# Performance work log

Measured on AMD Instinct MI355X. Metric: run time of the kernel, lower is better.

## Reference

```python
import jax, jax.numpy as jnp
import numpy as np

EPS = 1e-8
SIM_THRESHOLD = 0.5


def _conv(x, src, dst, W, b):
    # Gather per-edge endpoint features: x_j = source, x_i = target (PyG default flow)
    x_j = x[src]
    x_i = x[dst]
    # Cosine similarity per edge
    dot = jnp.sum(x_i * x_j, axis=1)
    denom = jnp.maximum(jnp.linalg.norm(x_i, axis=1) * jnp.linalg.norm(x_j, axis=1), EPS)
    sim = dot / denom
    mask = (sim > SIM_THRESHOLD).astype(x.dtype)[:, None]
    msg = x_j * mask
    # Scatter-add aggregate into target nodes
    agg = jax.ops.segment_sum(msg, dst, num_segments=x.shape[0])
    # update: Linear
    return agg @ W.T + b


def setup_inputs() -> dict:
    key = jax.random.key(0)
    k1, k2, k3, k4, k5 = jax.random.split(key, 5)
    N, E, D_IN, D_HID, D_OUT = 50000, 800000, 128, 256, 64
    x = jax.random.normal(k1, (N, D_IN), dtype=jnp.float32)
    edge_index = jax.random.randint(k2, (2, E), 0, N, dtype=jnp.int64)
    # Xavier-uniform linear weights, zero-ish bias
    lim1 = float(np.sqrt(6.0 / (D_IN + D_HID)))
    lim2 = float(np.sqrt(6.0 / (D_HID + D_OUT)))
    W1 = jax.random.uniform(k3, (D_HID, D_IN), minval=-lim1, maxval=lim1, dtype=jnp.float32)
    b1 = jnp.zeros((D_HID,), dtype=jnp.float32)
    W2 = jax.random.uniform(k4, (D_OUT, D_HID), minval=-lim2, maxval=lim2, dtype=jnp.float32)
    b2 = jnp.zeros((D_OUT,), dtype=jnp.float32)
    return {"x": x, "edge_index": edge_index, "W1": W1, "b1": b1, "W2": W2, "b2": b2}


def reference(x, edge_index, W1, b1, W2, b2):
    N = x.shape[0]
    # add self-loops
    loops = jnp.arange(N, dtype=edge_index.dtype)
    src = jnp.concatenate([edge_index[0], loops])
    dst = jnp.concatenate([edge_index[1], loops])
    h = _conv(x, src, dst, W1, b1)
    h = jax.nn.relu(h)  # dropout is identity in eval mode
    out = _conv(h, src, dst, W2, b2)
    return jax.nn.log_softmax(out, axis=-1)
```

## Files before the change

kernel.cpp:

```cpp
#include <hip/hip_runtime.h>
#include <math.h>

#define EPS 1e-8f
#define NB_SORT 256

#if defined(__has_builtin)
#if __has_builtin(__builtin_amdgcn_sdot4)
#define HAVE_SDOT4 1
#endif
#endif

typedef __attribute__((ext_vector_type(8))) short bf16x8;
typedef __attribute__((ext_vector_type(4))) float f32x4;

__device__ __forceinline__ int sdot4i(int a, int b, int c) {
#ifdef HAVE_SDOT4
  return __builtin_amdgcn_sdot4(a, b, c, false);
#else
  return c + ((int)(signed char)(a)) * ((int)(signed char)(b)) +
         ((int)(signed char)(a >> 8)) * ((int)(signed char)(b >> 8)) +
         ((int)(signed char)(a >> 16)) * ((int)(signed char)(b >> 16)) +
         (a >> 24) * (b >> 24);
#endif
}

__device__ __forceinline__ float wave_reduce_sum(float v) {
#pragma unroll
  for (int off = 32; off > 0; off >>= 1)
    v += __shfl_xor(v, off, 64);
  return v;
}

__device__ __forceinline__ float wave_reduce_max(float v) {
#pragma unroll
  for (int off = 32; off > 0; off >>= 1)
    v = fmaxf(v, __shfl_xor(v, off, 64));
  return v;
}

__device__ __forceinline__ float dot4(float4 a, float4 b) {
  return a.x * b.x + a.y * b.y + a.z * b.z + a.w * b.w;
}

__device__ __forceinline__ int clampq(float q) {
  int i = (int)rintf(q);
  return i < -127 ? -127 : (i > 127 ? 127 : i);
}

__device__ __forceinline__ void split_bf16(float x, unsigned int& hi,
                                           unsigned int& lo) {
  unsigned int u = __float_as_uint(x);
  hi = u >> 16;
  float hf = __uint_as_float(u & 0xFFFF0000u);
  float r = x - hf;
  lo = __float_as_uint(r) >> 16;
}

__device__ __forceinline__ void split8(float4 a0, float4 a1, bf16x8& th,
                                       bf16x8& tl) {
  unsigned int hh[8], ll[8];
  split_bf16(a0.x, hh[0], ll[0]); split_bf16(a0.y, hh[1], ll[1]);
  split_bf16(a0.z, hh[2], ll[2]); split_bf16(a0.w, hh[3], ll[3]);
  split_bf16(a1.x, hh[4], ll[4]); split_bf16(a1.y, hh[5], ll[5]);
  split_bf16(a1.z, hh[6], ll[6]); split_bf16(a1.w, hh[7], ll[7]);
#pragma unroll
  for (int j = 0; j < 8; ++j) {
    th[j] = (short)hh[j];
    tl[j] = (short)ll[j];
  }
}

__global__ __launch_bounds__(256) void hist_coarse(const int* __restrict__ dst,
                                                   int* __restrict__ hist_blk,
                                                   int E, int nbuck) {
  __shared__ int lh[1024];
  int t = threadIdx.x, blk = blockIdx.x;
  for (int i = t; i < nbuck; i += 256) lh[i] = 0;
  __syncthreads();
  int ch = (E + NB_SORT - 1) / NB_SORT;
  int lo = blk * ch, hi = min(E, lo + ch);
  for (int e = lo + t; e < hi; e += 256) atomicAdd(&lh[dst[e] >> 6], 1);
  __syncthreads();
  for (int i = t; i < nbuck; i += 256) hist_blk[i * NB_SORT + blk] = lh[i];
}

__global__ __launch_bounds__(256) void scan_local(int* __restrict__ hist,
                                                  int* __restrict__ bsum,
                                                  int nb) {
  __shared__ int tsum[256];
  int t = threadIdx.x;
  int base = blockIdx.x * 1024 + t * 4;
  int v0 = 0, v1 = 0, v2 = 0, v3 = 0;
  if (base + 3 < nb) {
    int4 q = *(const int4*)&hist[base];
    v0 = q.x; v1 = q.y; v2 = q.z; v3 = q.w;
  } else {
    if (base + 0 < nb) v0 = hist[base + 0];
    if (base + 1 < nb) v1 = hist[base + 1];
    if (base + 2 < nb) v2 = hist[base + 2];
  }
  tsum[t] = v0 + v1 + v2 + v3;
  __syncthreads();
  for (int off = 1; off < 256; off <<= 1) {
    int u = 0;
    if (t >= off) u = tsum[t - off];
    __syncthreads();
    if (t >= off) tsum[t] += u;
    __syncthreads();
  }
  int excl = (t == 0) ? 0 : tsum[t - 1];
  int e0 = excl, e1 = excl + v0, e2 = e1 + v1, e3 = e2 + v2;
  if (base + 3 < nb) {
    *(int4*)&hist[base] = make_int4(e0, e1, e2, e3);
  } else {
    if (base + 0 < nb) hist[base + 0] = e0;
    if (base + 1 < nb) hist[base + 1] = e1;
    if (base + 2 < nb) hist[base + 2] = e2;
  }
  if (t == 255) bsum[blockIdx.x] = tsum[255];
}

__global__ __launch_bounds__(256) void scan_bsum(int* __restrict__ bsum,
                                                 int nblk) {
  __shared__ int sh[256];
  int t = threadIdx.x;
  sh[t] = (t < nblk) ? bsum[t] : 0;
  __syncthreads();
  for (int off = 1; off < 256; off <<= 1) {
    int u = 0;
    if (t >= off) u = sh[t - off];
    __syncthreads();
    if (t >= off) sh[t] += u;
    __syncthreads();
  }
  if (t < nblk) bsum[t] = (t == 0) ? 0 : sh[t - 1];
}

__global__ __launch_bounds__(256) void add_bsum(int* __restrict__ hist,
                                                const int* __restrict__ bsum,
                                                int nb) {
  int i = blockIdx.x * blockDim.x + threadIdx.x;
  if (i < nb) hist[i] += bsum[i >> 10];
}

__global__ __launch_bounds__(256) void scatter_coarse(
    const int* __restrict__ src, const int* __restrict__ dst,
    const int* __restrict__ S, int2* __restrict__ epair, int E, int nbuck) {
  __shared__ int lb[1024];
  int t = threadIdx.x, blk = blockIdx.x;
  for (int i = t; i < nbuck; i += 256) lb[i] = S[i * NB_SORT + blk];
  __syncthreads();
  int ch = (E + NB_SORT - 1) / NB_SORT;
  int lo = blk * ch, hi = min(E, lo + ch);
  for (int e = lo + t; e < hi; e += 256) {
    int d = dst[e];
    int pos = atomicAdd(&lb[d >> 6], 1);
    epair[pos] = make_int2(src[e], d);
  }
}

__global__ __launch_bounds__(256) void fine_sort(
    const int2* __restrict__ epair, const int* __restrict__ S,
    int2* __restrict__ spair, int E, int nbuck) {
  __shared__ int fh[64];
  __shared__ int cur[64];
  int b = blockIdx.x, t = threadIdx.x;
  int bstart = S[b * NB_SORT];
  int bend = (b + 1 < nbuck) ? S[(b + 1) * NB_SORT] : E;
  if (t < 64) fh[t] = 0;
  __syncthreads();
  for (int e = bstart + t; e < bend; e += 256)
    atomicAdd(&fh[epair[e].y & 63], 1);
  __syncthreads();
  if (t < 64) {
    int v = fh[t];
    int incl = v;
#pragma unroll
    for (int off = 1; off < 64; off <<= 1) {
      int u = __shfl_up(incl, off, 64);
      if (t >= off) incl += u;
    }
    cur[t] = incl - v;
  }
  __syncthreads();
  for (int e = bstart + t; e < bend; e += 256) {
    int2 p = epair[e];
    int pos = atomicAdd(&cur[p.y & 63], 1);
    spair[bstart + pos] = p;
  }
}

__global__ __launch_bounds__(256) void prep_x(const float* __restrict__ x,
                                              signed char* __restrict__ qx,
                                              float4* __restrict__ nprop,
                                              float* __restrict__ agg,
                                              int N) {
  int node = (int)((blockIdx.x * blockDim.x + threadIdx.x) >> 6);
  int lane = threadIdx.x & 63;
  if (node >= N) return;
  float2 v = *(const float2*)(x + (size_t)node * 128 + lane * 2);
  float ax = fabsf(v.x), ay = fabsf(v.y);
  float mx = wave_reduce_max(fmaxf(ax, ay));
  float l1 = wave_reduce_sum(ax + ay);
  float ss = wave_reduce_sum(v.x * v.x + v.y * v.y);
  float s = mx * (1.0f / 127.0f);
  float inv = (mx > 0.f) ? 127.0f / mx : 0.f;
  int q0 = clampq(v.x * inv), q1 = clampq(v.y * inv);
  unsigned short w = (unsigned short)((q0 & 0xff) | ((q1 & 0xff) << 8));
  ((unsigned short*)(qx + (size_t)node * 128))[lane] = w;
  float l1q = s * wave_reduce_sum((float)(abs(q0) + abs(q1)));
  bool sp = ss > 0.5f * fmaxf(ss, EPS);
  *(float2*)(agg + (size_t)node * 128 + lane * 2) =
      sp ? v : make_float2(0.f, 0.f);
  if (lane == 0)
    nprop[node] = make_float4(sqrtf(ss), s, fmaxf(l1, l1q), 0.f);
}

__global__ __launch_bounds__(256) void prep_h(const float* __restrict__ h,
                                              signed char* __restrict__ qh,
                                              float4* __restrict__ nprop,
                                              float* __restrict__ agg,
                                              int N) {
  int node = (int)((blockIdx.x * blockDim.x + threadIdx.x) >> 6);
  int lane = threadIdx.x & 63;
  if (node >= N) return;
  float4 v = *(const float4*)(h + (size_t)node * 256 + lane * 4);
  float ax = fabsf(v.x), ay = fabsf(v.y), az = fabsf(v.z), aw = fabsf(v.w);
  float mx = wave_reduce_max(fmaxf(fmaxf(ax, ay), fmaxf(az, aw)));
  float l1 = wave_reduce_sum(ax + ay + az + aw);
  float ss = wave_reduce_sum(dot4(v, v));
  float s = mx * (1.0f / 127.0f);
  float inv = (mx > 0.f) ? 127.0f / mx : 0.f;
  int q0 = clampq(v.x * inv), q1 = clampq(v.y * inv);
  int q2 = clampq(v.z * inv), q3 = clampq(v.w * inv);
  int w = (q0 & 0xff) | ((q1 & 0xff) << 8) | ((q2 & 0xff) << 16) | (q3 << 24);
  ((int*)(qh + (size_t)node * 256))[lane] = w;
  float l1q = s * wave_reduce_sum((float)(abs(q0) + abs(q1) + abs(q2) + abs(q3)));
  bool sp = ss > 0.5f * fmaxf(ss, EPS);
  *(float4*)(agg + (size_t)node * 256 + lane * 4) =
      sp ? v : make_float4(0.f, 0.f, 0.f, 0.f);
  if (lane == 0)
    nprop[node] = make_float4(sqrtf(ss), s, fmaxf(l1, l1q), 0.f);
}

template <int D>
__global__ __launch_bounds__(256) void conv_coop(
    const float* __restrict__ xf, const signed char* __restrict__ qt,
    const float4* __restrict__ nprop, const int2* __restrict__ spair,
    float* __restrict__ agg, int E) {
  constexpr int G = D / 16;
  constexpr int EPW = 64 / G;
  constexpr int V = D / 64;
  const int tid = threadIdx.x;
  const int lane = tid & 63;
  const int wv = tid >> 6;
  const int g = lane & (G - 1);
  const int sub = lane / G;
  const int e = (blockIdx.x * 4 + wv) * EPW + sub;
  const bool valid = e < E;
  int2 p = spair[valid ? e : (E - 1)];
  const int s = p.x, d = p.y;
  float4 nps = nprop[s];
  float4 npd = nprop[d];
  int id = 0;
  {
    int4 a = *(const int4*)(qt + (size_t)s * D + g * 16);
    int4 bq = *(const int4*)(qt + (size_t)d * D + g * 16);
    id = sdot4i(a.x, bq.x, id);
    id = sdot4i(a.y, bq.y, id);
    id = sdot4i(a.z, bq.z, id);
    id = sdot4i(a.w, bq.w, id);
  }
#pragma unroll
  for (int off = G / 2; off > 0; off >>= 1) id += __shfl_xor(id, off, 64);
  float denom = fmaxf(nps.x * npd.x, EPS);
  float thr = 0.5f * denom;
  float approx = (nps.y * npd.y) * (float)id;
  float m = 0.5002f * (nps.y * npd.z + npd.y * nps.z) + 2e-6f * denom + 1e-7f;
  bool maybe = valid && (approx > thr - m);
  bool defp = maybe && (approx - m > thr);
  bool amb = maybe && !defp;
  unsigned long long defmask = __ballot(defp && g == 0);
  unsigned long long ambmask = __ballot(amb && g == 0);
  while (defmask) {
    int ln = __ffsll((long long)defmask) - 1;
    defmask &= defmask - 1;
    int es = __shfl(s, ln);
    int ed = __shfl(d, ln);
    float* arow = agg + (size_t)ed * D + lane * V;
    if constexpr (V == 2) {
      float2 a = *(const float2*)(xf + (size_t)es * D + lane * 2);
      atomicAdd(&arow[0], a.x);
      atomicAdd(&arow[1], a.y);
    } else {
      float4 a = *(const float4*)(xf + (size_t)es * D + lane * 4);
      atomicAdd(&arow[0], a.x);
      atomicAdd(&arow[1], a.y);
      atomicAdd(&arow[2], a.z);
      atomicAdd(&arow[3], a.w);
    }
  }
  while (ambmask) {
    int ln = __ffsll((long long)ambmask) - 1;
    ambmask &= ambmask - 1;
    int es = __shfl(s, ln);
    int ed = __shfl(d, ln);
    float nsx = __shfl(nps.x, ln);
    float ndx = __shfl(npd.x, ln);
    float sv[V], dvv[V];
    if constexpr (V == 2) {
      float2 a = *(const float2*)(xf + (size_t)es * D + lane * 2);
      float2 b = *(const float2*)(xf + (size_t)ed * D + lane * 2);
      sv[0] = a.x; sv[1] = a.y; dvv[0] = b.x; dvv[1] = b.y;
    } else {
      float4 a = *(const float4*)(xf + (size_t)es * D + lane * 4);
      float4 b = *(const float4*)(xf + (size_t)ed * D + lane * 4);
      sv[0] = a.x; sv[1] = a.y; sv[2] = a.z; sv[3] = a.w;
      dvv[0] = b.x; dvv[1] = b.y; dvv[2] = b.z; dvv[3] = b.w;
    }
    float dx = 0.f;
#pragma unroll
    for (int q = 0; q < V; ++q) dx += sv[q] * dvv[q];
    dx = wave_reduce_sum(dx);
    if (dx > 0.5f * fmaxf(nsx * ndx, EPS)) {
      float* arow = agg + (size_t)ed * D + lane * V;
#pragma unroll
      for (int q = 0; q < V; ++q) atomicAdd(&arow[q], sv[q]);
    }
  }
}

__global__ __launch_bounds__(256) void split_w(
    const float* __restrict__ W, unsigned short* __restrict__ Wh,
    unsigned short* __restrict__ Wl, int total4) {
  int i = blockIdx.x * 256 + threadIdx.x;
  if (i >= total4) return;
  float4 w = ((const float4*)W)[i];
  unsigned int h0, h1, h2, h3, l0, l1, l2, l3;
  split_bf16(w.x, h0, l0); split_bf16(w.y, h1, l1);
  split_bf16(w.z, h2, l2); split_bf16(w.w, h3, l3);
  ((uint2*)Wh)[i] = make_uint2(h0 | (h1 << 16), h2 | (h3 << 16));
  ((uint2*)Wl)[i] = make_uint2(l0 | (l1 << 16), l2 | (l3 << 16));
}

__global__ __launch_bounds__(256) void gemm1_mfma4(
    const float* __restrict__ A, const unsigned short* __restrict__ Wh,
    const unsigned short* __restrict__ Wl, const float* __restrict__ bias,
    float* __restrict__ C, int M, int nwg) {
  constexpr int K = 128, NN = 256;
  int orig = blockIdx.x;
  int qq = nwg >> 3, rr8 = nwg & 7;
  int xcd = orig & 7, loc = orig >> 3;
  int wg = (xcd < rr8 ? xcd * (qq + 1) : rr8 * (qq + 1) + (xcd - rr8) * qq) + loc;
  const int rowblk = wg >> 1, nblk = wg & 1;
  const int tid = threadIdx.x;
  const int lane = tid & 63;
  const int wv = tid >> 6;
  const int lrow = lane & 15, kg = lane >> 4;
  const int r0 = rowblk * 128 + wv * 32;
  const int n0 = nblk * 128;
  f32x4 acc[2][8] = {};

  for (int k0 = 0; k0 < K; k0 += 32) {
    bf16x8 ah[2], al[2];
#pragma unroll
    for (int m = 0; m < 2; ++m) {
      int row = r0 + m * 16 + lrow;
      const float* ap = A + (size_t)row * K + k0 + kg * 8;
      float4 a0 = *(const float4*)ap;
      float4 a1 = *(const float4*)(ap + 4);
      split8(a0, a1, ah[m], al[m]);
    }
    bf16x8 bh[8], bl[8];
#pragma unroll
    for (int n = 0; n < 8; ++n) {
      int wrow = n0 + n * 16 + lrow;
      bh[n] = *(const bf16x8*)&Wh[(size_t)wrow * K + k0 + kg * 8];
      bl[n] = *(const bf16x8*)&Wl[(size_t)wrow * K + k0 + kg * 8];
    }
#pragma unroll
    for (int m = 0; m < 2; ++m)
#pragma unroll
      for (int n = 0; n < 8; ++n) {
        acc[m][n] = __builtin_amdgcn_mfma_f32_16x16x32_bf16(ah[m], bh[n],
                                                            acc[m][n], 0, 0, 0);
        acc[m][n] = __builtin_amdgcn_mfma_f32_16x16x32_bf16(ah[m], bl[n],
                                                            acc[m][n], 0, 0, 0);
        acc[m][n] = __builtin_amdgcn_mfma_f32_16x16x32_bf16(al[m], bh[n],
                                                            acc[m][n], 0, 0, 0);
      }
  }

  float bv[8];
#pragma unroll
  for (int n = 0; n < 8; ++n) bv[n] = bias[n0 + n * 16 + lrow];
#pragma unroll
  for (int m = 0; m < 2; ++m)
#pragma unroll
    for (int r = 0; r < 4; ++r) {
      int orow = r0 + m * 16 + kg * 4 + r;
      if (orow < M) {
#pragma unroll
        for (int n = 0; n < 8; ++n) {
          float v = acc[m][n][r] + bv[n];
          C[(size_t)orow * NN + n0 + n * 16 + lrow] = fmaxf(v, 0.f);
        }
      }
    }
}

__global__ __launch_bounds__(256) void gemm2_mfma_lsm(
    const float* __restrict__ A, const unsigned short* __restrict__ Wh,
    const unsigned short* __restrict__ Wl, const float* __restrict__ bias,
    float* __restrict__ out, int M) {
  constexpr int K = 256;
  const int tid = threadIdx.x;
  const int lane = tid & 63;
  const int wv = tid >> 6;
  const int lrow = lane & 15, kg = lane >> 4;
  const int r0 = blockIdx.x * 128 + wv * 32;
  f32x4 acc[2][4] = {};

  for (int k0 = 0; k0 < K; k0 += 32) {
    bf16x8 ah[2], al[2];
#pragma unroll
    for (int m = 0; m < 2; ++m) {
      int row = r0 + m * 16 + lrow;
      const float* ap = A + (size_t)row * K + k0 + kg * 8;
      float4 a0 = *(const float4*)ap;
      float4 a1 = *(const float4*)(ap + 4);
      split8(a0, a1, ah[m], al[m]);
    }
    bf16x8 bh[4], bl[4];
#pragma unroll
    for (int n = 0; n < 4; ++n) {
      int wrow = n * 16 + lrow;
      bh[n] = *(const bf16x8*)&Wh[(size_t)wrow * K + k0 + kg * 8];
      bl[n] = *(const bf16x8*)&Wl[(size_t)wrow * K + k0 + kg * 8];
    }
#pragma unroll
    for (int m = 0; m < 2; ++m)
#pragma unroll
      for (int n = 0; n < 4; ++n) {
        acc[m][n] = __builtin_amdgcn_mfma_f32_16x16x32_bf16(ah[m], bh[n],
                                                            acc[m][n], 0, 0, 0);
        acc[m][n] = __builtin_amdgcn_mfma_f32_16x16x32_bf16(ah[m], bl[n],
                                                            acc[m][n], 0, 0, 0);
        acc[m][n] = __builtin_amdgcn_mfma_f32_16x16x32_bf16(al[m], bh[n],
                                                            acc[m][n], 0, 0, 0);
      }
  }

  float bv[4];
#pragma unroll
  for (int n = 0; n < 4; ++n) bv[n] = bias[n * 16 + lrow];
#pragma unroll
  for (int m = 0; m < 2; ++m)
#pragma unroll
    for (int r = 0; r < 4; ++r) {
      int row = r0 + m * 16 + kg * 4 + r;
      float v[4];
      float mx = -1e30f;
#pragma unroll
      for (int n = 0; n < 4; ++n) {
        v[n] = acc[m][n][r] + bv[n];
        mx = fmaxf(mx, v[n]);
      }
#pragma unroll
      for (int off = 8; off > 0; off >>= 1)
        mx = fmaxf(mx, __shfl_xor(mx, off, 64));
      float s = 0.f;
#pragma unroll
      for (int n = 0; n < 4; ++n) s += expf(v[n] - mx);
#pragma unroll
      for (int off = 8; off > 0; off >>= 1) s += __shfl_xor(s, off, 64);
      float lg = logf(s);
      if (row < M) {
#pragma unroll
        for (int n = 0; n < 4; ++n)
          out[(size_t)row * 64 + n * 16 + lrow] = v[n] - mx - lg;
      }
    }
}

extern "C" void kernel_launch(void* const* d_in, const int* in_sizes, int n_in,
                              void* d_out, int out_size, void* d_ws,
                              size_t ws_size, hipStream_t stream) {
  const float* x  = (const float*)d_in[0];
  const int* eidx = (const int*)d_in[1];
  const float* W1 = (const float*)d_in[2];
  const float* b1 = (const float*)d_in[3];
  const float* W2 = (const float*)d_in[4];
  const float* b2 = (const float*)d_in[5];
  float* out = (float*)d_out;

  const int N = in_sizes[0] / 128;
  const int E = in_sizes[1] / 2;
  const int* src = eidx;
  const int* dst = eidx + E;

  const int nbuck = (N + 63) / 64;
  const int ntot = nbuck * NB_SORT;
  const int nblk2 = (ntot + 1023) / 1024;

  float* agg    = (float*)d_ws;
  float* h      = agg + (size_t)N * 256;
  float4* npx   = (float4*)(h + (size_t)N * 256);
  float4* nph   = npx + N;
  int* S        = (int*)(nph + N);
  int* bsum     = S + ntot;
  int2* spair   = (int2*)(bsum + 256);
  signed char* qh = (signed char*)(spair + E);
  unsigned short* W2h = (unsigned short*)(qh + (size_t)N * 256);
  unsigned short* W2l = W2h + 64 * 256;
  unsigned short* W1h = W2l + 64 * 256;
  unsigned short* W1l = W1h + 256 * 128;
  int2* epair   = (int2*)h;
  signed char* qx = (signed char*)(h + (size_t)N * 64);

  split_w<<<16, 256, 0, stream>>>(W2, W2h, W2l, 64 * 256 / 4);
  split_w<<<32, 256, 0, stream>>>(W1, W1h, W1l, 256 * 128 / 4);

  hist_coarse<<<NB_SORT, 256, 0, stream>>>(dst, S, E, nbuck);
  scan_local<<<nblk2, 256, 0, stream>>>(S, bsum, ntot);
  scan_bsum<<<1, 256, 0, stream>>>(bsum, nblk2);
  add_bsum<<<(ntot + 255) / 256, 256, 0, stream>>>(S, bsum, ntot);
  scatter_coarse<<<NB_SORT, 256, 0, stream>>>(src, dst, S, epair, E, nbuck);
  fine_sort<<<nbuck, 256, 0, stream>>>(epair, S, spair, E, nbuck);

  prep_x<<<(N + 3) / 4, 256, 0, stream>>>(x, qx, npx, agg, N);
  conv_coop<128><<<(E + 31) / 32, 256, 0, stream>>>(x, qx, npx, spair, agg, E);
  const int nwg1 = ((N + 127) / 128) * 2;
  gemm1_mfma4<<<nwg1, 256, 0, stream>>>(agg, W1h, W1l, b1, h, N, nwg1);

  prep_h<<<(N + 3) / 4, 256, 0, stream>>>(h, qh, nph, agg, N);
  conv_coop<256><<<(E + 15) / 16, 256, 0, stream>>>(h, qh, nph, spair, agg, E);
  gemm2_mfma_lsm<<<dim3((N + 127) / 128), 256, 0, stream>>>(agg, W2h, W2l, b2,
                                                            out, N);
}
```

Measured before the change: 278.8 us.

## Fuse layer-2 node prep (quantize, norms, self-loop init) into GEMM1 epilogue

Removes the separate prep_h kernel by computing per-row max, L2 and L1 norms, int8 quantization, the self-loop aggregate and node properties inside the first GEMM's epilogue. GEMM1 is retiled so each block owns 32 full rows (the four waves split the 256 columns), with cross-wave reductions through shared memory. The aim is to avoid re-reading h and to drop one launch. In exchange the blocks are smaller, there are extra syncs, and stores become scalar per-element writes of h, agg2 and qh, which may coalesce poorly. Separate agg buffers are now used for the two layers.

```diff
diff --git a/kernel.cpp b/kernel.cpp
--- a/kernel.cpp
+++ b/kernel.cpp
@@ -212,33 +212,6 @@
   bool sp = ss > 0.5f * fmaxf(ss, EPS);
   *(float2*)(agg + (size_t)node * 128 + lane * 2) =
       sp ? v : make_float2(0.f, 0.f);
-  if (lane == 0)
-    nprop[node] = make_float4(sqrtf(ss), s, fmaxf(l1, l1q), 0.f);
-}
-
-__global__ __launch_bounds__(256) void prep_h(const float* __restrict__ h,
-                                              signed char* __restrict__ qh,
-                                              float4* __restrict__ nprop,
-                                              float* __restrict__ agg,
-                                              int N) {
-  int node = (int)((blockIdx.x * blockDim.x + threadIdx.x) >> 6);
-  int lane = threadIdx.x & 63;
-  if (node >= N) return;
-  float4 v = *(const float4*)(h + (size_t)node * 256 + lane * 4);
-  float ax = fabsf(v.x), ay = fabsf(v.y), az = fabsf(v.z), aw = fabsf(v.w);
-  float mx = wave_reduce_max(fmaxf(fmaxf(ax, ay), fmaxf(az, aw)));
-  float l1 = wave_reduce_sum(ax + ay + az + aw);
-  float ss = wave_reduce_sum(dot4(v, v));
-  float s = mx * (1.0f / 127.0f);
-  float inv = (mx > 0.f) ? 127.0f / mx : 0.f;
-  int q0 = clampq(v.x * inv), q1 = clampq(v.y * inv);
-  int q2 = clampq(v.z * inv), q3 = clampq(v.w * inv);
-  int w = (q0 & 0xff) | ((q1 & 0xff) << 8) | ((q2 & 0xff) << 16) | (q3 << 24);
-  ((int*)(qh + (size_t)node * 256))[lane] = w;
-  float l1q = s * wave_reduce_sum((float)(abs(q0) + abs(q1) + abs(q2) + abs(q3)));
-  bool sp = ss > 0.5f * fmaxf(ss, EPS);
-  *(float4*)(agg + (size_t)node * 256 + lane * 4) =
-      sp ? v : make_float4(0.f, 0.f, 0.f, 0.f);
   if (lane == 0)
     nprop[node] = make_float4(sqrtf(ss), s, fmaxf(l1, l1q), 0.f);
 }
@@ -343,24 +316,27 @@
   ((uint2*)Wl)[i] = make_uint2(l0 | (l1 << 16), l2 | (l3 << 16));
 }
 
-__global__ __launch_bounds__(256) void gemm1_mfma4(
+__global__ __launch_bounds__(256) void gemm1_prep_fused(
     const float* __restrict__ A, const unsigned short* __restrict__ Wh,
     const unsigned short* __restrict__ Wl, const float* __restrict__ bias,
-    float* __restrict__ C, int M, int nwg) {
+    float* __restrict__ h, signed char* __restrict__ qh,
+    float4* __restrict__ nprop, float* __restrict__ agg2, int M, int nwg) {
   constexpr int K = 128, NN = 256;
   int orig = blockIdx.x;
   int qq = nwg >> 3, rr8 = nwg & 7;
   int xcd = orig & 7, loc = orig >> 3;
   int wg = (xcd < rr8 ? xcd * (qq + 1) : rr8 * (qq + 1) + (xcd - rr8) * qq) + loc;
-  const int rowblk = wg >> 1, nblk = wg & 1;
   const int tid = threadIdx.x;
   const int lane = tid & 63;
   const int wv = tid >> 6;
   const int lrow = lane & 15, kg = lane >> 4;
-  const int r0 = rowblk * 128 + wv * 32;
-  const int n0 = nblk * 128;
-  f32x4 acc[2][8] = {};
-
+  const int r0 = wg * 32;
+  const int n0 = wv * 64;
+  __shared__ float4 red[32][4];
+  __shared__ float4 state[32];
+  __shared__ float red2[32][4];
+
+  f32x4 acc[2][4] = {};
   for (int k0 = 0; k0 < K; k0 += 32) {
     bf16x8 ah[2], al[2];
 #pragma unroll
@@ -371,9 +347,9 @@
       float4 a1 = *(const float4*)(ap + 4);
       split8(a0, a1, ah[m], al[m]);
     }
-    bf16x8 bh[8], bl[8];
-#pragma unroll
-    for (int n = 0; n < 8; ++n) {
+    bf16x8 bh[4], bl[4];
+#pragma unroll
+    for (int n = 0; n < 4; ++n) {
       int wrow = n0 + n * 16 + lrow;
       bh[n] = *(const bf16x8*)&Wh[(size_t)wrow * K + k0 + kg * 8];
       bl[n] = *(const bf16x8*)&Wl[(size_t)wrow * K + k0 + kg * 8];
@@ -381,7 +357,7 @@
 #pragma unroll
     for (int m = 0; m < 2; ++m)
 #pragma unroll
-      for (int n = 0; n < 8; ++n) {
+      for (int n = 0; n < 4; ++n) {
         acc[m][n] = __builtin_amdgcn_mfma_f32_16x16x32_bf16(ah[m], bh[n],
                                                             acc[m][n], 0, 0, 0);
         acc[m][n] = __builtin_amdgcn_mfma_f32_16x16x32_bf16(ah[m], bl[n],
@@ -391,22 +367,92 @@
       }
   }
 
-  float bv[8];
-#pragma unroll
-  for (int n = 0; n < 8; ++n) bv[n] = bias[n0 + n * 16 + lrow];
+  float bv[4];
+#pragma unroll
+  for (int n = 0; n < 4; ++n) bv[n] = bias[n0 + n * 16 + lrow];
 #pragma unroll
   for (int m = 0; m < 2; ++m)
 #pragma unroll
+    for (int n = 0; n < 4; ++n)
+#pragma unroll
+      for (int r = 0; r < 4; ++r)
+        acc[m][n][r] = fmaxf(acc[m][n][r] + bv[n], 0.f);
+
+#pragma unroll
+  for (int m = 0; m < 2; ++m)
+#pragma unroll
     for (int r = 0; r < 4; ++r) {
-      int orow = r0 + m * 16 + kg * 4 + r;
-      if (orow < M) {
-#pragma unroll
-        for (int n = 0; n < 8; ++n) {
-          float v = acc[m][n][r] + bv[n];
-          C[(size_t)orow * NN + n0 + n * 16 + lrow] = fmaxf(v, 0.f);
+      float mx = 0.f, ss = 0.f, l1 = 0.f;
+#pragma unroll
+      for (int n = 0; n < 4; ++n) {
+        float v = acc[m][n][r];
+        float a = fabsf(v);
+        mx = fmaxf(mx, a);
+        ss += v * v;
+        l1 += a;
+      }
+#pragma unroll
+      for (int off = 1; off < 16; off <<= 1) {
+        mx = fmaxf(mx, __shfl_xor(mx, off, 64));
+        ss += __shfl_xor(ss, off, 64);
+        l1 += __shfl_xor(l1, off, 64);
+      }
+      if (lrow == 0) red[m * 16 + kg * 4 + r][wv] = make_float4(mx, ss, l1, 0.f);
+    }
+  __syncthreads();
+  if (tid < 32) {
+    float mx = 0.f, ss = 0.f, l1 = 0.f;
+#pragma unroll
+    for (int w = 0; w < 4; ++w) {
+      float4 p = red[tid][w];
+      mx = fmaxf(mx, p.x);
+      ss += p.y;
+      l1 += p.z;
+    }
+    float s = mx * (1.0f / 127.0f);
+    float inv = (mx > 0.f) ? 127.0f / mx : 0.f;
+    state[tid] = make_float4(ss, s, inv, l1);
+  }
+  __syncthreads();
+
+#pragma unroll
+  for (int m = 0; m < 2; ++m)
+#pragma unroll
+    for (int r = 0; r < 4; ++r) {
+      int lr = m * 16 + kg * 4 + r;
+      int grow = r0 + lr;
+      float4 st = state[lr];
+      float inv = st.z;
+      float spm = (st.x > 0.5f * fmaxf(st.x, EPS)) ? 1.0f : 0.0f;
+      int sq = 0;
+      bool ok = grow < M;
+#pragma unroll
+      for (int n = 0; n < 4; ++n) {
+        float v = acc[m][n][r];
+        int q = clampq(v * inv);
+        sq += abs(q);
+        if (ok) {
+          int col = n0 + n * 16 + lrow;
+          h[(size_t)grow * NN + col] = v;
+          agg2[(size_t)grow * NN + col] = spm * v;
+          qh[(size_t)grow * NN + col] = (signed char)q;
         }
       }
-    }
+#pragma unroll
+      for (int off = 1; off < 16; off <<= 1) sq += __shfl_xor(sq, off, 64);
+      if (lrow == 0) red2[lr][wv] = (float)sq;
+    }
+  __syncthreads();
+  if (tid < 32) {
+    float sq = 0.f;
+#pragma unroll
+    for (int w = 0; w < 4; ++w) sq += red2[tid][w];
+    float4 st = state[tid];
+    float l1q = st.y * sq;
+    int grow = r0 + tid;
+    if (grow < M)
+      nprop[grow] = make_float4(sqrtf(st.x), st.y, fmaxf(st.w, l1q), 0.f);
+  }
 }
 
 __global__ __launch_bounds__(256) void gemm2_mfma_lsm(
@@ -503,8 +549,9 @@
   const int ntot = nbuck * NB_SORT;
   const int nblk2 = (ntot + 1023) / 1024;
 
-  float* agg    = (float*)d_ws;
-  float* h      = agg + (size_t)N * 256;
+  float* agg1   = (float*)d_ws;
+  float* agg2   = agg1 + (size_t)N * 128;
+  float* h      = agg2 + (size_t)N * 256;
   float4* npx   = (float4*)(h + (size_t)N * 256);
   float4* nph   = npx + N;
   int* S        = (int*)(nph + N);
@@ -528,13 +575,13 @@
   scatter_coarse<<<NB_SORT, 256, 0, stream>>>(src, dst, S, epair, E, nbuck);
   fine_sort<<<nbuck, 256, 0, stream>>>(epair, S, spair, E, nbuck);
 
-  prep_x<<<(N + 3) / 4, 256, 0, stream>>>(x, qx, npx, agg, N);
-  conv_coop<128><<<(E + 31) / 32, 256, 0, stream>>>(x, qx, npx, spair, agg, E);
-  const int nwg1 = ((N + 127) / 128) * 2;
-  gemm1_mfma4<<<nwg1, 256, 0, stream>>>(agg, W1h, W1l, b1, h, N, nwg1);
-
-  prep_h<<<(N + 3) / 4, 256, 0, stream>>>(h, qh, nph, agg, N);
-  conv_coop<256><<<(E + 15) / 16, 256, 0, stream>>>(h, qh, nph, spair, agg, E);
-  gemm2_mfma_lsm<<<dim3((N + 127) / 128), 256, 0, stream>>>(agg, W2h, W2l, b2,
+  prep_x<<<(N + 3) / 4, 256, 0, stream>>>(x, qx, npx, agg1, N);
+  conv_coop<128><<<(E + 31) / 32, 256, 0, stream>>>(x, qx, npx, spair, agg1, E);
+  const int nwg1 = (N + 31) / 32;
+  gemm1_prep_fused<<<nwg1, 256, 0, stream>>>(agg1, W1h, W1l, b1, h, qh, nph,
+                                             agg2, N, nwg1);
+
+  conv_coop<256><<<(E + 15) / 16, 256, 0, stream>>>(h, qh, nph, spair, agg2, E);
+  gemm2_mfma_lsm<<<dim3((N + 127) / 128), 256, 0, stream>>>(agg2, W2h, W2l, b2,
                                                             out, N);
 }
```

Result: faster. 265.4 us (-4.8%).
